# Kernel optimization log

Hardware: AMD Instinct MI355X
Metric: run time of the kernel (lower is better)

## Reference

```python
import jax, jax.numpy as jnp
import numpy as np

N, E, IN, HID, CLS = 40000, 640000, 128, 256, 40
K = 2  # SGConv k hops

def setup_inputs() -> dict:
    key = jax.random.key(0)
    ks = jax.random.split(key, 5)
    features = jax.random.normal(ks[0], (N, IN), dtype=jnp.float32)
    src = jax.random.randint(ks[1], (E,), 0, N)
    dst = jax.random.randint(ks[2], (E,), 0, N)
    # SGConv fc: in_feats -> n_hidden
    W1 = jax.random.normal(ks[3], (IN, HID), dtype=jnp.float32) / np.float32(np.sqrt(IN))
    b1 = jnp.zeros((HID,), dtype=jnp.float32)
    # model-level linear: n_hidden -> n_classes
    W2 = jax.random.normal(ks[4], (HID, CLS), dtype=jnp.float32) / np.float32(np.sqrt(HID))
    b2 = jnp.zeros((CLS,), dtype=jnp.float32)
    return {"features": features, "src": src, "dst": dst,
            "W1": W1, "b1": b1, "W2": W2, "b2": b2}

def reference(features, src, dst, W1, b1, W2, b2):
    # symmetric degree norm (DGL SGConv: in-degree, clamp min=1)
    deg = jax.ops.segment_sum(jnp.ones((E,), jnp.float32), dst, num_segments=N)
    norm = jax.lax.rsqrt(jnp.maximum(deg, 1.0))[:, None]  # [N,1]
    h = features
    for _ in range(K):
        h = h * norm
        h = jax.ops.segment_sum(h[src], dst, num_segments=N)  # A @ h via edge scatter
        h = h * norm
    h = h @ W1 + b1            # SGConv fc
    return jax.nn.relu(h) @ W2 + b2  # model relu + linear
```

## Files before the change

### kernel.cpp

```cpp
#include <hip/hip_runtime.h>

#define N_NODES 40000
#define N_EDGES 640000
#define IN_F 128
#define HID_F 256
#define CLS_F 40
#define CLS_P 48
#define MB 32
#define TS_LD 264

typedef __attribute__((ext_vector_type(8))) short bf16x8;
typedef __attribute__((ext_vector_type(4))) float f32x4;

#define MFMA(a, b, c) __builtin_amdgcn_mfma_f32_16x16x32_bf16(a, b, c, 0, 0, 0)

__device__ __forceinline__ unsigned short f32_to_bf16_rne(float f) {
    unsigned int u = __float_as_uint(f);
    unsigned int r = u + 0x7fffu + ((u >> 16) & 1u);
    return (unsigned short)(r >> 16);
}


__global__ void k_count(const int* __restrict__ dst, int* __restrict__ counts) {
    int e = blockIdx.x * blockDim.x + threadIdx.x;
    if (e < N_EDGES) atomicAdd(&counts[dst[e]], 1);
}

__global__ void k_scan1(const int* __restrict__ counts, int* __restrict__ bsum) {
    __shared__ int s[256];
    int i = blockIdx.x * 256 + threadIdx.x;
    s[threadIdx.x] = (i < N_NODES) ? counts[i] : 0;
    __syncthreads();
    for (int off = 128; off > 0; off >>= 1) {
        if (threadIdx.x < off) s[threadIdx.x] += s[threadIdx.x + off];
        __syncthreads();
    }
    if (threadIdx.x == 0) bsum[blockIdx.x] = s[0];
}

__global__ void k_scan2(int* __restrict__ bsum, int nb) {
    __shared__ int s[256];
    int t = threadIdx.x;
    int v = (t < nb) ? bsum[t] : 0;
    s[t] = v;
    __syncthreads();
    for (int off = 1; off < 256; off <<= 1) {
        int x = (t >= off) ? s[t - off] : 0;
        __syncthreads();
        s[t] += x;
        __syncthreads();
    }
    if (t < nb) bsum[t] = s[t] - v;
}

__global__ void k_scan3(const int* __restrict__ counts, const int* __restrict__ bsum,
                        int* __restrict__ rowptr, int* __restrict__ cursor) {
    __shared__ int s[256];
    int t = threadIdx.x;
    int i = blockIdx.x * 256 + t;
    int v = (i < N_NODES) ? counts[i] : 0;
    s[t] = v;
    __syncthreads();
    for (int off = 1; off < 256; off <<= 1) {
        int x = (t >= off) ? s[t - off] : 0;
        __syncthreads();
        s[t] += x;
        __syncthreads();
    }
    if (i < N_NODES) {
        int excl = s[t] - v + bsum[blockIdx.x];
        rowptr[i] = excl;
        cursor[i] = excl;
    }
}

__global__ void k_norm(const int* __restrict__ counts,
                       float* __restrict__ norm, float* __restrict__ norm2) {
    int i = blockIdx.x * blockDim.x + threadIdx.x;
    if (i < N_NODES) {
        float d = (float)counts[i];
        float r = rsqrtf(fmaxf(d, 1.0f));
        norm[i] = r;
        norm2[i] = r * r;
    }
}

__global__ void k_fill(const int* __restrict__ src, const int* __restrict__ dst,
                       int* __restrict__ cursor, int* __restrict__ csr_src) {
    int e = blockIdx.x * blockDim.x + threadIdx.x;
    if (e < N_EDGES) {
        int d = dst[e];
        int p = atomicAdd(&cursor[d], 1);
        csr_src[p] = src[e];
    }
}


__global__ __launch_bounds__(256) void k_prep(
        const float* __restrict__ W1, const float* __restrict__ W2,
        unsigned short* __restrict__ w1hi, unsigned short* __restrict__ w1lo,
        unsigned short* __restrict__ w2hi, unsigned short* __restrict__ w2lo) {
    int idx = blockIdx.x * 256 + threadIdx.x;
    if (idx < IN_F * HID_F) {
        int k = idx >> 8;
        int c = idx & 255;
        float v = W1[idx];
        unsigned short hi = f32_to_bf16_rne(v);
        float fh = __uint_as_float((unsigned)hi << 16);
        unsigned short lo = f32_to_bf16_rne(v - fh);
        w1hi[c * IN_F + k] = hi;
        w1lo[c * IN_F + k] = lo;
    }
    int idx2 = idx - IN_F * HID_F;
    if (idx2 >= 0 && idx2 < CLS_P * HID_F) {
        int c = idx2 >> 8;
        int k = idx2 & 255;
        float v = (c < CLS_F) ? W2[k * CLS_F + c] : 0.f;
        unsigned short hi = f32_to_bf16_rne(v);
        float fh = __uint_as_float((unsigned)hi << 16);
        unsigned short lo = f32_to_bf16_rne(v - fh);
        w2hi[c * HID_F + k] = hi;
        w2lo[c * HID_F + k] = lo;
    }
}


#define HOP_BODY(S0, S1, S2, S3)                                             \
    do {                                                                     \
        float c0 = scale[S0], c1 = scale[S1], c2 = scale[S2], c3 = scale[S3];\
        float4 v0 = ((const float4*)(gin + (size_t)(S0) * IN_F))[lane];      \
        float4 v1 = ((const float4*)(gin + (size_t)(S1) * IN_F))[lane];      \
        float4 v2 = ((const float4*)(gin + (size_t)(S2) * IN_F))[lane];      \
        float4 v3 = ((const float4*)(gin + (size_t)(S3) * IN_F))[lane];      \
        acc.x = fmaf(v0.x, c0, acc.x); acc.y = fmaf(v0.y, c0, acc.y);        \
        acc.z = fmaf(v0.z, c0, acc.z); acc.w = fmaf(v0.w, c0, acc.w);        \
        acc.x = fmaf(v1.x, c1, acc.x); acc.y = fmaf(v1.y, c1, acc.y);        \
        acc.z = fmaf(v1.z, c1, acc.z); acc.w = fmaf(v1.w, c1, acc.w);        \
        acc.x = fmaf(v2.x, c2, acc.x); acc.y = fmaf(v2.y, c2, acc.y);        \
        acc.z = fmaf(v2.z, c2, acc.z); acc.w = fmaf(v2.w, c2, acc.w);        \
        acc.x = fmaf(v3.x, c3, acc.x); acc.y = fmaf(v3.y, c3, acc.y);        \
        acc.z = fmaf(v3.z, c3, acc.z); acc.w = fmaf(v3.w, c3, acc.w);        \
    } while (0)

#define HOP_GATHER                                                           \
    float4 acc = make_float4(0.f, 0.f, 0.f, 0.f);                            \
    int i = 0;                                                               \
    int n0i = 0, n1i = 0, n2i = 0, n3i = 0;                                  \
    if (cnt >= 4) {                                                          \
        n0i = csr_src[start];     n1i = csr_src[start + 1];                  \
        n2i = csr_src[start + 2]; n3i = csr_src[start + 3];                  \
    }                                                                        \
    for (; i + 7 < cnt; i += 4) {                                            \
        int s0 = n0i, s1 = n1i, s2 = n2i, s3 = n3i;                          \
        n0i = csr_src[start + i + 4]; n1i = csr_src[start + i + 5];          \
        n2i = csr_src[start + i + 6]; n3i = csr_src[start + i + 7];          \
        HOP_BODY(s0, s1, s2, s3);                                            \
    }                                                                        \
    if (i + 3 < cnt) {                     \
        HOP_BODY(n0i, n1i, n2i, n3i);                                        \
        i += 4;                                                              \
    }                                                                        \
    for (; i < cnt; i++) {                                                   \
        int s = csr_src[start + i];                                          \
        float sc = scale[s];                                                 \
        float4 v = ((const float4*)(gin + (size_t)s * IN_F))[lane];          \
        acc.x = fmaf(v.x, sc, acc.x); acc.y = fmaf(v.y, sc, acc.y);          \
        acc.z = fmaf(v.z, sc, acc.z); acc.w = fmaf(v.w, sc, acc.w);          \
    }

__global__ __launch_bounds__(256) void k_hop(
        const float* __restrict__ gin, float* __restrict__ gout,
        const int* __restrict__ csr_src, const int* __restrict__ rowptr,
        const int* __restrict__ counts, const float* __restrict__ scale) {
    int gid  = blockIdx.x * 8 + (threadIdx.x >> 5);
    int lane = threadIdx.x & 31;
    if (gid >= N_NODES) return;
    int start = rowptr[gid];
    int cnt   = counts[gid];
    HOP_GATHER
    ((float4*)(gout + (size_t)gid * IN_F))[lane] = acc;
}

__global__ __launch_bounds__(256) void k_hop_split(
        const float* __restrict__ gin,
        unsigned short* __restrict__ ghi, unsigned short* __restrict__ glo,
        const int* __restrict__ csr_src, const int* __restrict__ rowptr,
        const int* __restrict__ counts, const float* __restrict__ scale,
        const float* __restrict__ norm) {
    int gid  = blockIdx.x * 8 + (threadIdx.x >> 5);
    int lane = threadIdx.x & 31;
    if (gid >= N_NODES) return;
    int start = rowptr[gid];
    int cnt   = counts[gid];
    HOP_GATHER
    float nrm = norm[gid];
    float vv[4] = {acc.x * nrm, acc.y * nrm, acc.z * nrm, acc.w * nrm};
    ushort4 h, l;
    unsigned short* hp = (unsigned short*)&h;
    unsigned short* lp = (unsigned short*)&l;
    #pragma unroll
    for (int j = 0; j < 4; j++) {
        unsigned short hi = f32_to_bf16_rne(vv[j]);
        float fh = __uint_as_float((unsigned)hi << 16);
        hp[j] = hi;
        lp[j] = f32_to_bf16_rne(vv[j] - fh);
    }
    ((ushort4*)(ghi + (size_t)gid * IN_F))[lane] = h;
    ((ushort4*)(glo + (size_t)gid * IN_F))[lane] = l;
}


#define LOAD_A(AH, AL, rt) do {                                              \
    const unsigned short* hp_ = h2hi + (size_t)(n0 + (rt) * 16 + lr) * IN_F + lg * 8; \
    const unsigned short* lp_ = h2lo + (size_t)(n0 + (rt) * 16 + lr) * IN_F + lg * 8; \
    _Pragma("unroll")                                                        \
    for (int kq = 0; kq < 4; kq++) {                                         \
        AH[kq] = *(const bf16x8*)(hp_ + kq * 32);                            \
        AL[kq] = *(const bf16x8*)(lp_ + kq * 32);                            \
    }                                                                        \
} while (0)

#define TILE(AH, AL, rt) do {                                                \
    _Pragma("unroll")                                                        \
    for (int ct = 0; ct < 4; ct++) {                                         \
        f32x4 acc = {0.f, 0.f, 0.f, 0.f};                                    \
        _Pragma("unroll")                                                    \
        for (int kq = 0; kq < 4; kq++) {                                     \
            acc = MFMA(AH[kq], b1h[ct][kq], acc);                            \
            acc = MFMA(AH[kq], b1l[ct][kq], acc);                            \
            acc = MFMA(AL[kq], b1h[ct][kq], acc);                            \
        }                                                                    \
        int col_ = w * 64 + ct * 16 + lr;                                    \
        _Pragma("unroll")                                                    \
        for (int r = 0; r < 4; r++) {                                        \
            int row_ = (rt) * 16 + lg * 4 + r;                               \
            float v_ = acc[r] + b1v[ct];                                     \
            v_ = v_ > 0.f ? v_ : 0.f;                                        \
            unsigned short hi_ = f32_to_bf16_rne(v_);                        \
            float fh_ = __uint_as_float((unsigned)hi_ << 16);                \
            tshi[row_ * TS_LD + col_] = hi_;                                 \
            tslo[row_ * TS_LD + col_] = f32_to_bf16_rne(v_ - fh_);           \
        }                                                                    \
    }                                                                        \
} while (0)

__global__ __launch_bounds__(256, 2) void k_mlp(
        const unsigned short* __restrict__ h2hi, const unsigned short* __restrict__ h2lo,
        const unsigned short* __restrict__ w1hi, const unsigned short* __restrict__ w1lo,
        const float* __restrict__ b1,
        const unsigned short* __restrict__ w2hi, const unsigned short* __restrict__ w2lo,
        const float* __restrict__ b2,
        float* __restrict__ out) {
    __shared__ __align__(16) unsigned short tshi[MB * TS_LD];
    __shared__ __align__(16) unsigned short tslo[MB * TS_LD];
    int n0 = blockIdx.x * MB;
    int t  = threadIdx.x;
    int w  = t >> 6;
    int l  = t & 63;
    int lr = l & 15;
    int lg = l >> 4;

    bf16x8 b1h[4][4], b1l[4][4];
    float  b1v[4];
    #pragma unroll
    for (int ct = 0; ct < 4; ct++) {
        int col = w * 64 + ct * 16 + lr;
        const unsigned short* bhp = w1hi + (size_t)col * IN_F + lg * 8;
        const unsigned short* blp = w1lo + (size_t)col * IN_F + lg * 8;
        #pragma unroll
        for (int kq = 0; kq < 4; kq++) {
            b1h[ct][kq] = *(const bf16x8*)(bhp + kq * 32);
            b1l[ct][kq] = *(const bf16x8*)(blp + kq * 32);
        }
        b1v[ct] = b1[col];
    }

    bf16x8 aAh[4], aAl[4], aBh[4], aBl[4];
    LOAD_A(aAh, aAl, 0);
    LOAD_A(aBh, aBl, 1);
    TILE(aAh, aAl, 0);
    TILE(aBh, aBl, 1);
    __syncthreads();

    if (w < 3) {
        int col = w * 16 + lr;
        bf16x8 b2h[8], b2l[8];
        const unsigned short* bhp = w2hi + (size_t)col * HID_F + lg * 8;
        const unsigned short* blp = w2lo + (size_t)col * HID_F + lg * 8;
        #pragma unroll
        for (int kk = 0; kk < 8; kk++) {
            b2h[kk] = *(const bf16x8*)(bhp + kk * 32);
            b2l[kk] = *(const bf16x8*)(blp + kk * 32);
        }
        float bias = (col < CLS_F) ? b2[col] : 0.f;
        #pragma unroll
        for (int rt2 = 0; rt2 < 2; rt2++) {
            const unsigned short* ahp = tshi + (rt2 * 16 + lr) * TS_LD + lg * 8;
            const unsigned short* alp = tslo + (rt2 * 16 + lr) * TS_LD + lg * 8;
            f32x4 acc0 = {0.f, 0.f, 0.f, 0.f};
            f32x4 acc1 = {0.f, 0.f, 0.f, 0.f};
            #pragma unroll
            for (int kk = 0; kk < 4; kk++) {
                bf16x8 a_h0 = *(const bf16x8*)(ahp + kk * 32);
                bf16x8 a_l0 = *(const bf16x8*)(alp + kk * 32);
                bf16x8 a_h1 = *(const bf16x8*)(ahp + (kk + 4) * 32);
                bf16x8 a_l1 = *(const bf16x8*)(alp + (kk + 4) * 32);
                acc0 = MFMA(a_h0, b2h[kk], acc0);
                acc1 = MFMA(a_h1, b2h[kk + 4], acc1);
                acc0 = MFMA(a_h0, b2l[kk], acc0);
                acc1 = MFMA(a_h1, b2l[kk + 4], acc1);
                acc0 = MFMA(a_l0, b2h[kk], acc0);
                acc1 = MFMA(a_l1, b2h[kk + 4], acc1);
            }
            if (col < CLS_F) {
                #pragma unroll
                for (int r = 0; r < 4; r++) {
                    int mrow = n0 + rt2 * 16 + lg * 4 + r;
                    out[(size_t)mrow * CLS_F + col] = acc0[r] + acc1[r] + bias;
                }
            }
        }
    }
}


extern "C" void kernel_launch(void* const* d_in, const int* in_sizes, int n_in,
                              void* d_out, int out_size, void* d_ws, size_t ws_size,
                              hipStream_t stream) {
    const float* features = (const float*)d_in[0];
    const int*   src      = (const int*)d_in[1];
    const int*   dst      = (const int*)d_in[2];
    const float* W1       = (const float*)d_in[3];
    const float* b1       = (const float*)d_in[4];
    const float* W2       = (const float*)d_in[5];
    const float* b2       = (const float*)d_in[6];
    float*       out      = (float*)d_out;

    char* ws = (char*)d_ws;
    size_t off = 0;
    auto alloc = [&](size_t bytes) -> void* {
        void* p = ws + off;
        off += (bytes + 255) & ~(size_t)255;
        return p;
    };
    int*   counts = (int*)alloc((size_t)N_NODES * 4);
    int*   rowptr = (int*)alloc((size_t)N_NODES * 4);
    int*   cursor = (int*)alloc((size_t)N_NODES * 4);
    int*   bsum   = (int*)alloc(256 * 4);
    float* norm   = (float*)alloc((size_t)N_NODES * 4);
    float* norm2  = (float*)alloc((size_t)N_NODES * 4);
    int*   csr    = (int*)alloc((size_t)N_EDGES * 4);
    float* h1     = (float*)alloc((size_t)N_NODES * IN_F * 4);
    unsigned short* h2hi = (unsigned short*)alloc((size_t)N_NODES * IN_F * 2);
    unsigned short* h2lo = (unsigned short*)alloc((size_t)N_NODES * IN_F * 2);
    unsigned short* w1hi = (unsigned short*)alloc((size_t)HID_F * IN_F * 2);
    unsigned short* w1lo = (unsigned short*)alloc((size_t)HID_F * IN_F * 2);
    unsigned short* w2hi = (unsigned short*)alloc((size_t)CLS_P * HID_F * 2);
    unsigned short* w2lo = (unsigned short*)alloc((size_t)CLS_P * HID_F * 2);

    hipMemsetAsync(counts, 0, (size_t)N_NODES * 4, stream);

    int nb = (N_NODES + 255) / 256;
    k_count<<<(N_EDGES + 255) / 256, 256, 0, stream>>>(dst, counts);
    k_prep<<<(IN_F * HID_F + CLS_P * HID_F + 255) / 256, 256, 0, stream>>>(
        W1, W2, w1hi, w1lo, w2hi, w2lo);
    k_scan1<<<nb, 256, 0, stream>>>(counts, bsum);
    k_scan2<<<1, 256, 0, stream>>>(bsum, nb);
    k_scan3<<<nb, 256, 0, stream>>>(counts, bsum, rowptr, cursor);
    k_norm<<<nb, 256, 0, stream>>>(counts, norm, norm2);
    k_fill<<<(N_EDGES + 255) / 256, 256, 0, stream>>>(src, dst, cursor, csr);

    k_hop<<<(N_NODES + 7) / 8, 256, 0, stream>>>(features, h1, csr, rowptr, counts, norm);
    k_hop_split<<<(N_NODES + 7) / 8, 256, 0, stream>>>(h1, h2hi, h2lo, csr, rowptr, counts,
                                                       norm2, norm);

    k_mlp<<<N_NODES / MB, 256, 0, stream>>>(h2hi, h2lo, w1hi, w1lo, b1, w2hi, w2lo, b2, out);
}
```

Baseline: 269.2 us.

## Slice feature dimension in gather hops and prescale features by norm

Each aggregation hop is split into 8 feature slices of 16 floats, with 4 threads per node and 64 nodes per block, so concurrently running blocks touch a narrower column band of the source matrix. The aim is better L2 locality for random neighbor gathers. A new pre-pass multiplies the features by norm so the first hop skips the per-edge scale load. The next hop's input scale is folded into the previous hop's output (norm2), so the inner loop becomes plain adds. The trade-offs are an extra full read and write of the feature matrix, and CSR indices being re-read once per slice.

```diff
diff --git a/kernel.cpp b/kernel.cpp
--- a/kernel.cpp
+++ b/kernel.cpp
@@ -8,6 +8,8 @@
 #define CLS_P 48
 #define MB 32
 #define TS_LD 264
+#define SLICES 8
+#define SLICE_F 16
 
 typedef __attribute__((ext_vector_type(8))) short bf16x8;
 typedef __attribute__((ext_vector_type(4))) float f32x4;
@@ -93,6 +95,80 @@
         int p = atomicAdd(&cursor[d], 1);
         csr_src[p] = src[e];
     }
+}
+
+
+__global__ __launch_bounds__(256) void k_scale(
+        const float* __restrict__ f, const float* __restrict__ norm,
+        float* __restrict__ xs) {
+    int i = blockIdx.x * 256 + threadIdx.x;
+    float4 v = ((const float4*)f)[i];
+    float s = norm[i >> 5];
+    v.x *= s; v.y *= s; v.z *= s; v.w *= s;
+    ((float4*)xs)[i] = v;
+}
+
+
+#define HOP_SLICED_GATHER                                                     \
+    int slice = blockIdx.x & (SLICES - 1);                                    \
+    int chunk = blockIdx.x >> 3;                                              \
+    int t   = threadIdx.x;                                                    \
+    int gid = chunk * 64 + (t >> 2);     \
+    int ln  = t & 3;                                                          \
+    int start = rowptr[gid];                                                  \
+    int cnt   = counts[gid];                                                  \
+    const float* base = gin + slice * SLICE_F + ln * 4;                       \
+    float4 acc = make_float4(0.f, 0.f, 0.f, 0.f);                             \
+    int i = 0;                                                                \
+    for (; i + 3 < cnt; i += 4) {                                             \
+        int s0 = csr_src[start + i];     int s1 = csr_src[start + i + 1];     \
+        int s2 = csr_src[start + i + 2]; int s3 = csr_src[start + i + 3];     \
+        float4 v0 = *(const float4*)(base + (size_t)s0 * IN_F);               \
+        float4 v1 = *(const float4*)(base + (size_t)s1 * IN_F);               \
+        float4 v2 = *(const float4*)(base + (size_t)s2 * IN_F);               \
+        float4 v3 = *(const float4*)(base + (size_t)s3 * IN_F);               \
+        acc.x += v0.x + v1.x + v2.x + v3.x;                                   \
+        acc.y += v0.y + v1.y + v2.y + v3.y;                                   \
+        acc.z += v0.z + v1.z + v2.z + v3.z;                                   \
+        acc.w += v0.w + v1.w + v2.w + v3.w;                                   \
+    }                                                                         \
+    for (; i < cnt; i++) {                                                    \
+        int s = csr_src[start + i];                                           \
+        float4 v = *(const float4*)(base + (size_t)s * IN_F);                 \
+        acc.x += v.x; acc.y += v.y; acc.z += v.z; acc.w += v.w;               \
+    }
+
+__global__ __launch_bounds__(256) void k_hop(
+        const float* __restrict__ gin, float* __restrict__ gout,
+        const int* __restrict__ csr_src, const int* __restrict__ rowptr,
+        const int* __restrict__ counts, const float* __restrict__ oscale) {
+    HOP_SLICED_GATHER
+    float sc = oscale[gid];
+    acc.x *= sc; acc.y *= sc; acc.z *= sc; acc.w *= sc;
+    *(float4*)(gout + (size_t)gid * IN_F + slice * SLICE_F + ln * 4) = acc;
+}
+
+__global__ __launch_bounds__(256) void k_hop_split(
+        const float* __restrict__ gin,
+        unsigned short* __restrict__ ghi, unsigned short* __restrict__ glo,
+        const int* __restrict__ csr_src, const int* __restrict__ rowptr,
+        const int* __restrict__ counts, const float* __restrict__ oscale) {
+    HOP_SLICED_GATHER
+    float sc = oscale[gid];
+    float vv[4] = {acc.x * sc, acc.y * sc, acc.z * sc, acc.w * sc};
+    ushort4 h, l;
+    unsigned short* hp = (unsigned short*)&h;
+    unsigned short* lp = (unsigned short*)&l;
+    #pragma unroll
+    for (int j = 0; j < 4; j++) {
+        unsigned short hi = f32_to_bf16_rne(vv[j]);
+        float fh = __uint_as_float((unsigned)hi << 16);
+        hp[j] = hi;
+        lp[j] = f32_to_bf16_rne(vv[j] - fh);
+    }
+    size_t off = (size_t)gid * IN_F + slice * SLICE_F + ln * 4;
+    *(ushort4*)(ghi + off) = h;
+    *(ushort4*)(glo + off) = l;
 }
 
 
@@ -122,91 +198,6 @@
         w2hi[c * HID_F + k] = hi;
         w2lo[c * HID_F + k] = lo;
     }
-}
-
-
-#define HOP_BODY(S0, S1, S2, S3)                                             \
-    do {                                                                     \
-        float c0 = scale[S0], c1 = scale[S1], c2 = scale[S2], c3 = scale[S3];\
-        float4 v0 = ((const float4*)(gin + (size_t)(S0) * IN_F))[lane];      \
-        float4 v1 = ((const float4*)(gin + (size_t)(S1) * IN_F))[lane];      \
-        float4 v2 = ((const float4*)(gin + (size_t)(S2) * IN_F))[lane];      \
-        float4 v3 = ((const float4*)(gin + (size_t)(S3) * IN_F))[lane];      \
-        acc.x = fmaf(v0.x, c0, acc.x); acc.y = fmaf(v0.y, c0, acc.y);        \
-        acc.z = fmaf(v0.z, c0, acc.z); acc.w = fmaf(v0.w, c0, acc.w);        \
-        acc.x = fmaf(v1.x, c1, acc.x); acc.y = fmaf(v1.y, c1, acc.y);        \
-        acc.z = fmaf(v1.z, c1, acc.z); acc.w = fmaf(v1.w, c1, acc.w);        \
-        acc.x = fmaf(v2.x, c2, acc.x); acc.y = fmaf(v2.y, c2, acc.y);        \
-        acc.z = fmaf(v2.z, c2, acc.z); acc.w = fmaf(v2.w, c2, acc.w);        \
-        acc.x = fmaf(v3.x, c3, acc.x); acc.y = fmaf(v3.y, c3, acc.y);        \
-        acc.z = fmaf(v3.z, c3, acc.z); acc.w = fmaf(v3.w, c3, acc.w);        \
-    } while (0)
-
-#define HOP_GATHER                                                           \
-    float4 acc = make_float4(0.f, 0.f, 0.f, 0.f);                            \
-    int i = 0;                                                               \
-    int n0i = 0, n1i = 0, n2i = 0, n3i = 0;                                  \
-    if (cnt >= 4) {                                                          \
-        n0i = csr_src[start];     n1i = csr_src[start + 1];                  \
-        n2i = csr_src[start + 2]; n3i = csr_src[start + 3];                  \
-    }                                                                        \
-    for (; i + 7 < cnt; i += 4) {                                            \
-        int s0 = n0i, s1 = n1i, s2 = n2i, s3 = n3i;                          \
-        n0i = csr_src[start + i + 4]; n1i = csr_src[start + i + 5];          \
-        n2i = csr_src[start + i + 6]; n3i = csr_src[start + i + 7];          \
-        HOP_BODY(s0, s1, s2, s3);                                            \
-    }                                                                        \
-    if (i + 3 < cnt) {                     \
-        HOP_BODY(n0i, n1i, n2i, n3i);                                        \
-        i += 4;                                                              \
-    }                                                                        \
-    for (; i < cnt; i++) {                                                   \
-        int s = csr_src[start + i];                                          \
-        float sc = scale[s];                                                 \
-        float4 v = ((const float4*)(gin + (size_t)s * IN_F))[lane];          \
-        acc.x = fmaf(v.x, sc, acc.x); acc.y = fmaf(v.y, sc, acc.y);          \
-        acc.z = fmaf(v.z, sc, acc.z); acc.w = fmaf(v.w, sc, acc.w);          \
-    }
-
-__global__ __launch_bounds__(256) void k_hop(
-        const float* __restrict__ gin, float* __restrict__ gout,
-        const int* __restrict__ csr_src, const int* __restrict__ rowptr,
-        const int* __restrict__ counts, const float* __restrict__ scale) {
-    int gid  = blockIdx.x * 8 + (threadIdx.x >> 5);
-    int lane = threadIdx.x & 31;
-    if (gid >= N_NODES) return;
-    int start = rowptr[gid];
-    int cnt   = counts[gid];
-    HOP_GATHER
-    ((float4*)(gout + (size_t)gid * IN_F))[lane] = acc;
-}
-
-__global__ __launch_bounds__(256) void k_hop_split(
-        const float* __restrict__ gin,
-        unsigned short* __restrict__ ghi, unsigned short* __restrict__ glo,
-        const int* __restrict__ csr_src, const int* __restrict__ rowptr,
-        const int* __restrict__ counts, const float* __restrict__ scale,
-        const float* __restrict__ norm) {
-    int gid  = blockIdx.x * 8 + (threadIdx.x >> 5);
-    int lane = threadIdx.x & 31;
-    if (gid >= N_NODES) return;
-    int start = rowptr[gid];
-    int cnt   = counts[gid];
-    HOP_GATHER
-    float nrm = norm[gid];
-    float vv[4] = {acc.x * nrm, acc.y * nrm, acc.z * nrm, acc.w * nrm};
-    ushort4 h, l;
-    unsigned short* hp = (unsigned short*)&h;
-    unsigned short* lp = (unsigned short*)&l;
-    #pragma unroll
-    for (int j = 0; j < 4; j++) {
-        unsigned short hi = f32_to_bf16_rne(vv[j]);
-        float fh = __uint_as_float((unsigned)hi << 16);
-        hp[j] = hi;
-        lp[j] = f32_to_bf16_rne(vv[j] - fh);
-    }
-    ((ushort4*)(ghi + (size_t)gid * IN_F))[lane] = h;
-    ((ushort4*)(glo + (size_t)gid * IN_F))[lane] = l;
 }
 
 
@@ -350,6 +341,7 @@
     float* norm   = (float*)alloc((size_t)N_NODES * 4);
     float* norm2  = (float*)alloc((size_t)N_NODES * 4);
     int*   csr    = (int*)alloc((size_t)N_EDGES * 4);
+    float* xs     = (float*)alloc((size_t)N_NODES * IN_F * 4);
     float* h1     = (float*)alloc((size_t)N_NODES * IN_F * 4);
     unsigned short* h2hi = (unsigned short*)alloc((size_t)N_NODES * IN_F * 2);
     unsigned short* h2lo = (unsigned short*)alloc((size_t)N_NODES * IN_F * 2);
@@ -370,9 +362,10 @@
     k_norm<<<nb, 256, 0, stream>>>(counts, norm, norm2);
     k_fill<<<(N_EDGES + 255) / 256, 256, 0, stream>>>(src, dst, cursor, csr);
 
-    k_hop<<<(N_NODES + 7) / 8, 256, 0, stream>>>(features, h1, csr, rowptr, counts, norm);
-    k_hop_split<<<(N_NODES + 7) / 8, 256, 0, stream>>>(h1, h2hi, h2lo, csr, rowptr, counts,
-                                                       norm2, norm);
+    k_scale<<<N_NODES * (IN_F / 4) / 256, 256, 0, stream>>>(features, norm, xs);
+    k_hop<<<SLICES * (N_NODES / 64), 256, 0, stream>>>(xs, h1, csr, rowptr, counts, norm2);
+    k_hop_split<<<SLICES * (N_NODES / 64), 256, 0, stream>>>(h1, h2hi, h2lo, csr, rowptr,
+                                                             counts, norm);
 
     k_mlp<<<N_NODES / MB, 256, 0, stream>>>(h2hi, h2lo, w1hi, w1lo, b1, w2hi, w2lo, b2, out);
 }
```

Measured after the change: 300.4 us. 11.6% more time.
